# Kernel optimization log

Measured on AMD Instinct MI355X. Metric: run time of the kernel, lower is better.

Reference implementation:

```python
import jax, jax.numpy as jnp
import numpy as np

N_GRAPHS = 128
NODES_PER_GRAPH = 512
N = N_GRAPHS * NODES_PER_GRAPH  # 65536 total nodes
C = 512        # num_channels
H = 8          # num_heads
HID = C // 2   # 256


def setup_inputs() -> dict:
    key = jax.random.key(0)
    k_x, k_t, k_w1, k_w2 = jax.random.split(key, 4)
    inputs = jax.random.normal(k_x, (N, C), dtype=jnp.float32)
    n_node = jnp.full((N_GRAPHS,), NODES_PER_GRAPH, dtype=jnp.int32)  # sums to N
    task = jax.random.randint(k_t, (N_GRAPHS,), 0, H, dtype=jnp.int32)
    # lecun_normal: std = 1/sqrt(fan_in)
    W1 = jax.random.normal(k_w1, (H, C, HID), dtype=jnp.float32) / np.sqrt(C)
    b1 = jnp.zeros((H, HID), dtype=jnp.float32)
    W2 = jax.random.normal(k_w2, (H, HID, 1), dtype=jnp.float32) / np.sqrt(HID)
    b2 = jnp.zeros((H, 1), dtype=jnp.float32)
    return {"inputs": inputs, "n_node": n_node, "task": task,
            "W1": W1, "b1": b1, "W2": W2, "b2": b2}


def reference(inputs, n_node, task, W1, b1, W2, b2):
    n = inputs.shape[0]
    # per-node head id (same as repeating kernel[head] by n_node, but cheap)
    head = jnp.repeat(task, n_node, total_repeat_length=n)  # [N]
    # layer 1: grouped matmul = all-head GEMM then per-node head selection
    h_all = jnp.einsum('ni,hio->nho', inputs, W1)            # [N, H, HID]
    h = jnp.take_along_axis(h_all, head[:, None, None], axis=1)[:, 0]  # [N, HID]
    h = h + b1[head]
    h = jax.nn.silu(h)
    # layer 2: out_features == 1, so direct per-node dot with gathered weights
    y = jnp.einsum('nc,nc->n', h, W2[head, :, 0])[:, None] + b2[head]  # [N, 1]
    return y
```

## Files before the change

### kernel.cpp

```cpp
#include <hip/hip_runtime.h>
#include <hip/hip_bf16.h>
#include <stdint.h>

typedef __bf16 bf16_t;
typedef __bf16 bf16x8 __attribute__((ext_vector_type(8)));
typedef float  f32x4  __attribute__((ext_vector_type(4)));

#define NGRAPH 128
#define NPG    512
#define CIN    512
#define HID    256
#define BM     64
#define BK     64

__device__ __forceinline__ void gl2lds16(const void* g, void* l) {
  __builtin_amdgcn_global_load_lds(
      (const __attribute__((address_space(1))) uint32_t*)g,
      (__attribute__((address_space(3))) uint32_t*)l, 16, 0, 0);
}

__global__ __launch_bounds__(256) void prep_w1(const float* __restrict__ W1,
                                               bf16_t* __restrict__ Bimg) {
  __shared__ float tile[64][65];
  const int n0 = blockIdx.x * 64;
  const int kt = blockIdx.y;
  const int h  = blockIdx.z;
  const int k0 = kt * 64;
  const int tid = threadIdx.x;
  const int r = tid >> 4, c4 = tid & 15;
  const float* src = W1 + (((size_t)h * CIN + k0) * HID + n0);
#pragma unroll
  for (int i = 0; i < 4; i++) {
    const int rr = r + i * 16;
    const float4 v = *(const float4*)(src + (size_t)rr * HID + c4 * 4);
    tile[rr][c4 * 4 + 0] = v.x; tile[rr][c4 * 4 + 1] = v.y;
    tile[rr][c4 * 4 + 2] = v.z; tile[rr][c4 * 4 + 3] = v.w;
  }
  __syncthreads();
  bf16_t* dst = Bimg + (size_t)(h * 8 + kt) * 16384;
#pragma unroll
  for (int i = 0; i < 2; i++) {
    const int u = tid + i * 256;
    const int n = u >> 3, c = u & 7;
    bf16x8 o;
#pragma unroll
    for (int j = 0; j < 8; j++) o[j] = (bf16_t)tile[c * 8 + j][n];
    const int ng = n0 + n;
    const int cp = c ^ (ng & 7);
    *(bf16x8*)(dst + (size_t)ng * 64 + cp * 8) = o;
  }
}

__global__ __launch_bounds__(256, 3) void energy_main(
    const float* __restrict__ x, const int* __restrict__ task,
    const bf16_t* __restrict__ Bimg, const float* __restrict__ b1,
    const float* __restrict__ W2, const float* __restrict__ b2,
    float* __restrict__ out) {
  __shared__ float  As[BM * BK];
  __shared__ bf16_t Bs[HID * BK];
  __shared__ float  red[4][BM];

  const int bx   = blockIdx.x;
  const int g    = bx >> 3;
  const int mt   = bx & 7;
  const int head = task[g];
  const int base = g * NPG + mt * BM;
  const int tid  = threadIdx.x;
  const int wave = tid >> 6, lane = tid & 63;
  const int q = lane >> 4, t = lane & 15;

  const float*  Ag = x + (size_t)base * CIN;
  const bf16_t* Bh = Bimg + (size_t)head * 8 * 16384;

  const int a_row16 = tid >> 4;
  const int a_cp    = tid & 15;

  f32x4 acc[4][4] = {};

  for (int kt = 0; kt < 8; kt++) {
    const int k0 = kt * 64;
    if (kt) __syncthreads();
#pragma unroll
    for (int j = 0; j < 4; j++) {
      const int row = j * 16 + a_row16;
      const int c = a_cp ^ (row & 7);
      gl2lds16(Ag + (size_t)row * CIN + k0 + c * 4, As + j * 1024 + tid * 4);
    }
    const bf16_t* Bt = Bh + (size_t)kt * 16384;
#pragma unroll
    for (int j = 0; j < 8; j++)
      gl2lds16(Bt + j * 2048 + tid * 8, Bs + j * 2048 + tid * 8);
    __syncthreads();

#pragma unroll
    for (int ks = 0; ks < 64; ks += 32) {
      bf16x8 bfr[4];
#pragma unroll
      for (int ni = 0; ni < 4; ni++) {
        const int n = wave * 64 + ni * 16 + t;
        const int cp = (ks / 8 + q) ^ (n & 7);
        bfr[ni] = *(const bf16x8*)(Bs + n * 64 + cp * 8);
      }
#pragma unroll
      for (int mi = 0; mi < 4; mi++) {
        const int row = mi * 16 + t;
        const int s = row & 7;
        const int c0 = ks / 4 + q * 2;
        const float4 v0 = *(const float4*)(As + row * 64 + ((c0) ^ s) * 4);
        const float4 v1 = *(const float4*)(As + row * 64 + ((c0 + 1) ^ s) * 4);
        bf16x8 af;
        af[0] = (bf16_t)v0.x; af[1] = (bf16_t)v0.y;
        af[2] = (bf16_t)v0.z; af[3] = (bf16_t)v0.w;
        af[4] = (bf16_t)v1.x; af[5] = (bf16_t)v1.y;
        af[6] = (bf16_t)v1.z; af[7] = (bf16_t)v1.w;
#pragma unroll
        for (int ni = 0; ni < 4; ni++)
          acc[mi][ni] = __builtin_amdgcn_mfma_f32_16x16x32_bf16(
              af, bfr[ni], acc[mi][ni], 0, 0, 0);
      }
    }
  }

  float w2c[4], b1c[4];
#pragma unroll
  for (int ni = 0; ni < 4; ni++) {
    const int col = wave * 64 + ni * 16 + t;
    w2c[ni] = W2[head * HID + col];
    b1c[ni] = b1[head * HID + col];
  }
  float part[4][4];
#pragma unroll
  for (int mi = 0; mi < 4; mi++)
#pragma unroll
    for (int r = 0; r < 4; r++) {
      float sacc = 0.f;
#pragma unroll
      for (int ni = 0; ni < 4; ni++) {
        const float hh = acc[mi][ni][r] + b1c[ni];
        sacc += (hh / (1.f + __expf(-hh))) * w2c[ni];
      }
      part[mi][r] = sacc;
    }
#pragma unroll
  for (int off = 1; off < 16; off <<= 1)
#pragma unroll
    for (int mi = 0; mi < 4; mi++)
#pragma unroll
      for (int r = 0; r < 4; r++)
        part[mi][r] += __shfl_xor(part[mi][r], off, 64);
  if (t == 0) {
#pragma unroll
    for (int mi = 0; mi < 4; mi++)
#pragma unroll
      for (int r = 0; r < 4; r++)
        red[wave][mi * 16 + q * 4 + r] = part[mi][r];
  }
  __syncthreads();
  if (tid < BM) {
    out[base + tid] = red[0][tid] + red[1][tid] + red[2][tid] + red[3][tid] +
                      b2[head];
  }
}

extern "C" void kernel_launch(void* const* d_in, const int* in_sizes, int n_in,
                              void* d_out, int out_size, void* d_ws,
                              size_t ws_size, hipStream_t stream) {
  const float* x    = (const float*)d_in[0];
  const int*   task = (const int*)d_in[2];
  const float* W1   = (const float*)d_in[3];
  const float* b1   = (const float*)d_in[4];
  const float* W2   = (const float*)d_in[5];
  const float* b2   = (const float*)d_in[6];
  float* out = (float*)d_out;

  bf16_t* Bimg = (bf16_t*)d_ws;

  prep_w1<<<dim3(4, 8, 8), 256, 0, stream>>>(W1, Bimg);
  energy_main<<<dim3(NGRAPH * 8), 256, 0, stream>>>(x, task, Bimg, b1, W2, b2,
                                                    out);
}
```

Measured before the change: 215.1 us.

## Prepack W1 into MFMA fragment layout and load B directly to registers

The weight-prep kernel now writes W1 in per-wave MFMA fragment order, so the main kernel loads B operands straight from global memory into registers instead of staging them through LDS. Removing the 32 KB B tile from shared memory allows occupancy to go from 3 to 4 blocks per CU. The K-tile order is also rotated per block to spread concurrent accesses across memory channels. The trade-off is more global/L2 traffic per wave for B and more registers held for the fragments, and the prep kernel now runs on fewer blocks with a serial loop.

```diff
diff --git a/kernel.cpp b/kernel.cpp
--- a/kernel.cpp
+++ b/kernel.cpp
@@ -20,45 +20,46 @@
 }
 
 __global__ __launch_bounds__(256) void prep_w1(const float* __restrict__ W1,
-                                               bf16_t* __restrict__ Bimg) {
+                                               bf16_t* __restrict__ Bfrag) {
   __shared__ float tile[64][65];
-  const int n0 = blockIdx.x * 64;
-  const int kt = blockIdx.y;
-  const int h  = blockIdx.z;
-  const int k0 = kt * 64;
+  const int kt = blockIdx.x;
+  const int h  = blockIdx.y;
   const int tid = threadIdx.x;
-  const int r = tid >> 4, c4 = tid & 15;
-  const float* src = W1 + (((size_t)h * CIN + k0) * HID + n0);
+  const int kr = tid >> 4, n4 = tid & 15;
+  for (int w = 0; w < 4; w++) {
+    if (w) __syncthreads();
+    const float* src = W1 + (((size_t)h * CIN + kt * 64) * HID + w * 64);
 #pragma unroll
-  for (int i = 0; i < 4; i++) {
-    const int rr = r + i * 16;
-    const float4 v = *(const float4*)(src + (size_t)rr * HID + c4 * 4);
-    tile[rr][c4 * 4 + 0] = v.x; tile[rr][c4 * 4 + 1] = v.y;
-    tile[rr][c4 * 4 + 2] = v.z; tile[rr][c4 * 4 + 3] = v.w;
-  }
-  __syncthreads();
-  bf16_t* dst = Bimg + (size_t)(h * 8 + kt) * 16384;
+    for (int i = 0; i < 4; i++) {
+      const int k = kr + i * 16;
+      const float4 v = *(const float4*)(src + (size_t)k * HID + n4 * 4);
+      tile[k][n4 * 4 + 0] = v.x; tile[k][n4 * 4 + 1] = v.y;
+      tile[k][n4 * 4 + 2] = v.z; tile[k][n4 * 4 + 3] = v.w;
+    }
+    __syncthreads();
+    bf16_t* dst = Bfrag + (size_t)(((h * 8 + kt) * 4 + w)) * 4096;
 #pragma unroll
-  for (int i = 0; i < 2; i++) {
-    const int u = tid + i * 256;
-    const int n = u >> 3, c = u & 7;
-    bf16x8 o;
+    for (int e = 0; e < 2; e++) {
+      const int idx = tid * 2 + e;
+      const int f = idx >> 6, lane = idx & 63;
+      const int ni = f >> 1, ks2 = f & 1;
+      const int q = lane >> 4, t = lane & 15;
+      bf16x8 o;
 #pragma unroll
-    for (int j = 0; j < 8; j++) o[j] = (bf16_t)tile[c * 8 + j][n];
-    const int ng = n0 + n;
-    const int cp = c ^ (ng & 7);
-    *(bf16x8*)(dst + (size_t)ng * 64 + cp * 8) = o;
+      for (int j = 0; j < 8; j++)
+        o[j] = (bf16_t)tile[ks2 * 32 + q * 8 + j][ni * 16 + t];
+      *(bf16x8*)(dst + (size_t)(f * 64 + lane) * 8) = o;
+    }
   }
 }
 
-__global__ __launch_bounds__(256, 3) void energy_main(
+__global__ __launch_bounds__(256, 4) void energy_main(
     const float* __restrict__ x, const int* __restrict__ task,
-    const bf16_t* __restrict__ Bimg, const float* __restrict__ b1,
+    const bf16_t* __restrict__ Bfrag, const float* __restrict__ b1,
     const float* __restrict__ W2, const float* __restrict__ b2,
     float* __restrict__ out) {
-  __shared__ float  As[BM * BK];
-  __shared__ bf16_t Bs[HID * BK];
-  __shared__ float  red[4][BM];
+  __shared__ float As[BM * BK];
+  __shared__ float red[4][BM];
 
   const int bx   = blockIdx.x;
   const int g    = bx >> 3;
@@ -70,42 +71,38 @@
   const int q = lane >> 4, t = lane & 15;
 
   const float*  Ag = x + (size_t)base * CIN;
-  const bf16_t* Bh = Bimg + (size_t)head * 8 * 16384;
+  const bf16_t* Bw = Bfrag + (size_t)(head * 32 + wave) * 4096;
 
   const int a_row16 = tid >> 4;
   const int a_cp    = tid & 15;
+  const int phase   = (bx * 5 + (bx >> 8)) & 7;
 
   f32x4 acc[4][4] = {};
 
-  for (int kt = 0; kt < 8; kt++) {
+  for (int kk = 0; kk < 8; kk++) {
+    const int kt = (kk + phase) & 7;
     const int k0 = kt * 64;
-    if (kt) __syncthreads();
+    if (kk) __syncthreads();
 #pragma unroll
     for (int j = 0; j < 4; j++) {
       const int row = j * 16 + a_row16;
       const int c = a_cp ^ (row & 7);
       gl2lds16(Ag + (size_t)row * CIN + k0 + c * 4, As + j * 1024 + tid * 4);
     }
-    const bf16_t* Bt = Bh + (size_t)kt * 16384;
+    const bf16_t* Bt = Bw + (size_t)kt * 16384;
+    bf16x8 bfr[8];
 #pragma unroll
-    for (int j = 0; j < 8; j++)
-      gl2lds16(Bt + j * 2048 + tid * 8, Bs + j * 2048 + tid * 8);
+    for (int f = 0; f < 8; f++)
+      bfr[f] = *(const bf16x8*)(Bt + (size_t)f * 512 + lane * 8);
     __syncthreads();
 
 #pragma unroll
-    for (int ks = 0; ks < 64; ks += 32) {
-      bf16x8 bfr[4];
-#pragma unroll
-      for (int ni = 0; ni < 4; ni++) {
-        const int n = wave * 64 + ni * 16 + t;
-        const int cp = (ks / 8 + q) ^ (n & 7);
-        bfr[ni] = *(const bf16x8*)(Bs + n * 64 + cp * 8);
-      }
+    for (int ks2 = 0; ks2 < 2; ks2++) {
 #pragma unroll
       for (int mi = 0; mi < 4; mi++) {
         const int row = mi * 16 + t;
         const int s = row & 7;
-        const int c0 = ks / 4 + q * 2;
+        const int c0 = ks2 * 8 + q * 2;
         const float4 v0 = *(const float4*)(As + row * 64 + ((c0) ^ s) * 4);
         const float4 v1 = *(const float4*)(As + row * 64 + ((c0 + 1) ^ s) * 4);
         bf16x8 af;
@@ -116,7 +113,7 @@
 #pragma unroll
         for (int ni = 0; ni < 4; ni++)
           acc[mi][ni] = __builtin_amdgcn_mfma_f32_16x16x32_bf16(
-              af, bfr[ni], acc[mi][ni], 0, 0, 0);
+              af, bfr[ni * 2 + ks2], acc[mi][ni], 0, 0, 0);
       }
     }
   }
@@ -173,9 +170,9 @@
   const float* b2   = (const float*)d_in[6];
   float* out = (float*)d_out;
 
-  bf16_t* Bimg = (bf16_t*)d_ws;
+  bf16_t* Bfrag = (bf16_t*)d_ws;
 
-  prep_w1<<<dim3(4, 8, 8), 256, 0, stream>>>(W1, Bimg);
-  energy_main<<<dim3(NGRAPH * 8), 256, 0, stream>>>(x, task, Bimg, b1, W2, b2,
+  prep_w1<<<dim3(8, 8), 256, 0, stream>>>(W1, Bfrag);
+  energy_main<<<dim3(NGRAPH * 8), 256, 0, stream>>>(x, task, Bfrag, b1, W2, b2,
                                                     out);
 }
```

Measured after the change: 219.0 us. Within noise of the previous version (+1.8%).
